# Optimization experiments

Hardware: AMD Instinct MI355X
Metric: run time of the kernel (lower is better)

## Reference

```python
import jax, jax.numpy as jnp
import numpy as np

DIM = 1536
NH = 12
HD = DIM // NH          # 128
C = HD // 2             # 64 rotary pairs
F, H, W = 6, 20, 20
L = F * H * W           # 2400
B = 1
MAX_POS = 1024
EPS = 1e-6


def _rope_freqs():
    """[MAX_POS, C, 2, 2] rotation matrices, split [22,21,21] across f/h/w axes."""
    c0 = C - 2 * (C // 3)           # 22
    c1 = C // 3                      # 21
    pos = np.arange(MAX_POS, dtype=np.float32)
    parts = []
    for m in (c0, c1, c1):
        inv = 1.0 / (10000.0 ** (np.arange(m, dtype=np.float32) / m))
        parts.append(pos[:, None] * inv[None, :])
    ang = np.concatenate(parts, axis=1)          # [MAX_POS, C]
    cos, sin = np.cos(ang), np.sin(ang)
    # R[..., j, k]: rows [cos, -sin], [sin, cos]
    R = np.stack([np.stack([cos, -sin], -1), np.stack([sin, cos], -1)], -2)
    return jnp.asarray(R, dtype=jnp.float32)


def setup_inputs() -> dict:
    key = jax.random.key(0)
    ks = jax.random.split(key, 12)
    s = 1.0 / np.sqrt(DIM)
    lin = lambda k: (jax.random.normal(k, (DIM, DIM), jnp.float32) * s)
    return {
        "x": jax.random.normal(ks[0], (B, L, DIM), jnp.float32),
        "Wq": lin(ks[1]), "bq": jax.random.normal(ks[2], (DIM,), jnp.float32) * 0.01,
        "Wk": lin(ks[3]), "bk": jax.random.normal(ks[4], (DIM,), jnp.float32) * 0.01,
        "Wv": lin(ks[5]), "bv": jax.random.normal(ks[6], (DIM,), jnp.float32) * 0.01,
        "Wo": lin(ks[7]), "bo": jax.random.normal(ks[8], (DIM,), jnp.float32) * 0.01,
        "gq": jnp.ones((DIM,), jnp.float32),
        "gk": jnp.ones((DIM,), jnp.float32),
        "seq_lens": jnp.full((B,), L, dtype=jnp.int32),
        "grid_sizes": jnp.asarray([[F, H, W]], dtype=jnp.int32),
        "freqs": _rope_freqs(),
    }


def _rms_norm(x, g, eps=EPS):
    # WanRMSNorm: x * rsqrt(mean(x^2, -1) + eps) * weight
    return x * jax.lax.rsqrt(jnp.mean(jnp.square(x), axis=-1, keepdims=True) + eps) * g


def _rope_apply(xh, grid_sizes, freqs):
    """xh: [B, L, n, d]; freqs: [MAX_POS, c, 2, 2]. All samples share one grid."""
    b, l, n, d = xh.shape
    c = d // 2
    c0 = c - 2 * (c // 3)
    c1 = c // 3
    f, h, w = (int(v) for v in np.asarray(grid_sizes[0]))
    # build per-position 3D rotation matrices: [f*h*w, c, 2, 2]
    fa = jnp.broadcast_to(freqs[:f, :c0][:, None, None], (f, h, w, c0, 2, 2))
    fb = jnp.broadcast_to(freqs[:h, c0:c0 + c1][None, :, None], (f, h, w, c1, 2, 2))
    fc = jnp.broadcast_to(freqs[:w, c0 + c1:c][None, None, :], (f, h, w, c1, 2, 2))
    R = jnp.concatenate([fa, fb, fc], axis=3).reshape(f * h * w, c, 2, 2)
    xp = xh.reshape(b, l, n, c, 2)
    out = jnp.einsum('lcjk,blnck->blncj', R, xp)
    return out.reshape(b, l, n, d)


def reference(x, Wq, bq, Wk, bk, Wv, bv, Wo, bo, gq, gk, seq_lens, grid_sizes, freqs):
    b, l = x.shape[:2]
    q = _rms_norm(x @ Wq.T + bq, gq).reshape(b, l, NH, HD)
    k = _rms_norm(x @ Wk.T + bk, gk).reshape(b, l, NH, HD)
    v = (x @ Wv.T + bv).reshape(b, l, NH, HD)
    q = _rope_apply(q, grid_sizes, freqs)
    k = _rope_apply(k, grid_sizes, freqs)
    # full attention with key-length mask (window_size=(-1,-1))
    scores = jnp.einsum('bqnd,bknd->bnqk', q, k) / np.sqrt(HD)
    kmask = jnp.arange(l)[None, :] < seq_lens[:, None]          # [B, L]
    scores = jnp.where(kmask[:, None, None, :], scores, -1e9)
    attn = jax.nn.softmax(scores, axis=-1)
    out = jnp.einsum('bnqk,bknd->bqnd', attn, v).reshape(b, l, DIM)
    return out @ Wo.T + bo
```

## Files before the change

### kernel.cpp

```cpp
#include <hip/hip_runtime.h>
#include <hip/hip_bf16.h>
#include <stdint.h>


#define DIM  1536
#define NH   12
#define HD   128
#define LSEQ 2400
#define LPAD 2432
#define KT2  32
#define NT2  (LPAD / KT2)

typedef __attribute__((ext_vector_type(8))) short short8;
typedef __attribute__((ext_vector_type(8))) _Float16 half8;
typedef __attribute__((ext_vector_type(4))) float f32x4;
typedef unsigned short ushort_t;
typedef unsigned int   uint32;

__device__ __forceinline__ ushort_t f2bf(float f) {
  union { float f; unsigned u; } v; v.f = f;
  unsigned r = (v.u + 0x7fffu + ((v.u >> 16) & 1u)) >> 16;
  return (ushort_t)r;
}
__device__ __forceinline__ float bf2f(ushort_t h) {
  union { unsigned u; float f; } v; v.u = ((unsigned)h) << 16;
  return v.f;
}
__device__ __forceinline__ uint32 cvtpk(float lo, float hi) {
  uint32 r;
  asm("v_cvt_pk_bf16_f32 %0, %1, %2" : "=v"(r) : "v"(lo), "v"(hi));
  return r;
}
__device__ __forceinline__ void async16(void* lds, const void* g) {
  __builtin_amdgcn_global_load_lds(
      (const __attribute__((address_space(1))) uint32*)g,
      (__attribute__((address_space(3))) uint32*)lds, 16, 0, 0);
}
__device__ __forceinline__ uint4 pack8(const float* f) {
  uint4 u;
  u.x = (uint32)f2bf(f[0]) | ((uint32)f2bf(f[1]) << 16);
  u.y = (uint32)f2bf(f[2]) | ((uint32)f2bf(f[3]) << 16);
  u.z = (uint32)f2bf(f[4]) | ((uint32)f2bf(f[5]) << 16);
  u.w = (uint32)f2bf(f[6]) | ((uint32)f2bf(f[7]) << 16);
  return u;
}

__global__ void cvt_all(const float* __restrict__ x,
                        const float* __restrict__ W0, const float* __restrict__ W1,
                        const float* __restrict__ W2, const float* __restrict__ W3,
                        ushort_t* __restrict__ xd,
                        ushort_t* __restrict__ d0, ushort_t* __restrict__ d1,
                        ushort_t* __restrict__ d2, ushort_t* __restrict__ d3)
{
  const int z = blockIdx.y;
  const int i = blockIdx.x * 256 + threadIdx.x;
  if (z == 0) {
    uint4 u = {0, 0, 0, 0};
    if (i * 8 < LSEQ * DIM) {
      float f[8];
      *(float4*)f = *(const float4*)(x + i * 8);
      *(float4*)(f + 4) = *(const float4*)(x + i * 8 + 4);
      u = pack8(f);
    }
    *(uint4*)(xd + i * 8) = u;
    return;
  }
  if (blockIdx.x >= DIM * DIM / 2048) return;
  const float* s = (z == 1) ? W0 : ((z == 2) ? W1 : ((z == 3) ? W2 : W3));
  ushort_t* d    = (z == 1) ? d0 : ((z == 2) ? d1 : ((z == 3) ? d2 : d3));
  float f[8];
  *(float4*)f = *(const float4*)(s + i * 8);
  *(float4*)(f + 4) = *(const float4*)(s + i * 8 + 4);
  *(uint4*)(d + i * 8) = pack8(f);
}

__global__ __launch_bounds__(256) void gemm_bt(
    const ushort_t* __restrict__ Ap,
    const ushort_t* __restrict__ B0, const ushort_t* __restrict__ B1, const ushort_t* __restrict__ B2,
    const float* __restrict__ b0, const float* __restrict__ b1, const float* __restrict__ b2,
    ushort_t* __restrict__ D0, ushort_t* __restrict__ D1, ushort_t* __restrict__ D2)
{
  const int z = blockIdx.y;
  const ushort_t* Bw  = (z == 0) ? B0 : ((z == 1) ? B1 : B2);
  const float* bias   = (z == 0) ? b0 : ((z == 1) ? b1 : b2);
  ushort_t* D         = (z == 0) ? D0 : ((z == 1) ? D1 : D2);

  const int bid = blockIdx.x;
  const int x_ = bid & 7, k_ = bid >> 3;
  const int swz = (x_ < 4 ? x_ * 29 : 116 + (x_ - 4) * 28) + k_;
  const int bm = swz / 12, bn = swz % 12;
  const int tid = threadIdx.x;
  const int w = tid >> 6, lam = tid & 63;
  const int wr = w >> 1, wc = w & 1;
  const int lane15 = lam & 15, quad = lam >> 4;

  __shared__ __align__(16) char lds[65536];

  f32x4 acc[4][4];
#pragma unroll
  for (int i = 0; i < 4; ++i)
#pragma unroll
    for (int j = 0; j < 4; ++j) acc[i][j] = {};

  const int sm = (w * 32) + (lam >> 3);
  const int sc = (lam & 7);

#define GSTAGE(k0, buf)                                                       \
  {                                                                           \
    char* sA_ = lds + (buf) * 32768;                                          \
    char* sB_ = lds + (buf) * 32768 + 16384;                                  \
    _Pragma("unroll")                                                         \
    for (int i = 0; i < 4; ++i) {                                             \
      const int li = w * 4096 + i * 1024;                                     \
      const int m = sm + i * 8;                                               \
      const int c = sc ^ (m & 7);                                             \
      async16(sA_ + li, Ap + (size_t)(bm * 128 + m) * DIM + (k0) + c * 8);    \
      async16(sB_ + li, Bw + (size_t)(bn * 128 + m) * DIM + (k0) + c * 8);    \
    }                                                                         \
  }

  GSTAGE(0, 0)
  __syncthreads();

  for (int t = 0; t < DIM / 64; ++t) {
    if (t + 1 < DIM / 64) GSTAGE((t + 1) * 64, (t + 1) & 1)
    const char* sA = lds + (t & 1) * 32768;
    const char* sB = lds + (t & 1) * 32768 + 16384;
#pragma unroll
    for (int kc = 0; kc < 2; ++kc) {
      const int chunk = kc * 4 + quad;
      short8 af[4], bfr[4];
#pragma unroll
      for (int i = 0; i < 4; ++i) {
        const int m = wr * 64 + i * 16 + lane15;
        af[i] = *(const short8*)(sA + m * 128 + ((chunk ^ (m & 7)) * 16));
      }
#pragma unroll
      for (int j = 0; j < 4; ++j) {
        const int n = wc * 64 + j * 16 + lane15;
        bfr[j] = *(const short8*)(sB + n * 128 + ((chunk ^ (n & 7)) * 16));
      }
#pragma unroll
      for (int i = 0; i < 4; ++i)
#pragma unroll
        for (int j = 0; j < 4; ++j)
          acc[i][j] = __builtin_amdgcn_mfma_f32_16x16x32_bf16(af[i], bfr[j], acc[i][j], 0, 0, 0);
    }
    __syncthreads();
  }
#undef GSTAGE

#pragma unroll
  for (int j = 0; j < 4; ++j) {
    const int n = bn * 128 + wc * 64 + j * 16 + lane15;
    const float bv = bias[n];
#pragma unroll
    for (int i = 0; i < 4; ++i) {
      const int mb = bm * 128 + wr * 64 + i * 16 + quad * 4;
#pragma unroll
      for (int r = 0; r < 4; ++r) {
        const int m = mb + r;
        D[(size_t)m * DIM + n] = f2bf(acc[i][j][r] + bv);
      }
    }
  }
}

__global__ __launch_bounds__(256) void gemm_o(
    const ushort_t* __restrict__ Ap, const ushort_t* __restrict__ Bw,
    const float* __restrict__ bias, float* __restrict__ D, int Mout)
{
  const int bid = blockIdx.x;
  const int swz = (bid & 7) * 57 + (bid >> 3);
  const int bm = swz / 12, bn = swz % 12;
  const int tid = threadIdx.x;
  const int w = tid >> 6, lam = tid & 63;
  const int wr = w >> 1, wc = w & 1;
  const int lane15 = lam & 15, quad = lam >> 4;

  __shared__ __align__(16) char lds[49152];

  f32x4 acc[2][4];
#pragma unroll
  for (int i = 0; i < 2; ++i)
#pragma unroll
    for (int j = 0; j < 4; ++j) acc[i][j] = {};

#define OSTAGE(k0, buf)                                                       \
  {                                                                           \
    char* sA_ = lds + (buf) * 24576;                                          \
    char* sB_ = lds + (buf) * 24576 + 8192;                                   \
    _Pragma("unroll")                                                         \
    for (int i = 0; i < 2; ++i) {                                             \
      const int slot = i * 256 + tid;           \
      const int row = slot >> 3;                                              \
      const int c = (slot & 7) ^ (row & 7);                                   \
      async16(sA_ + slot * 16, Ap + (size_t)(bm * 64 + row) * DIM + (k0) + c * 8); \
    }                                                                         \
    _Pragma("unroll")                                                         \
    for (int i = 0; i < 4; ++i) {                                             \
      const int slot = i * 256 + tid;            \
      const int row = slot >> 3;                                              \
      const int c = (slot & 7) ^ (row & 7);                                   \
      async16(sB_ + slot * 16, Bw + (size_t)(bn * 128 + row) * DIM + (k0) + c * 8); \
    }                                                                         \
  }

  OSTAGE(0, 0)
  __syncthreads();

  for (int t = 0; t < DIM / 64; ++t) {
    if (t + 1 < DIM / 64) OSTAGE((t + 1) * 64, (t + 1) & 1)
    const char* sA = lds + (t & 1) * 24576;
    const char* sB = lds + (t & 1) * 24576 + 8192;
#pragma unroll
    for (int kc = 0; kc < 2; ++kc) {
      const int chunk = kc * 4 + quad;
      short8 af[2], bfr[4];
#pragma unroll
      for (int i = 0; i < 2; ++i) {
        const int m = wr * 32 + i * 16 + lane15;
        af[i] = *(const short8*)(sA + m * 128 + ((chunk ^ (m & 7)) * 16));
      }
#pragma unroll
      for (int j = 0; j < 4; ++j) {
        const int n = wc * 64 + j * 16 + lane15;
        bfr[j] = *(const short8*)(sB + n * 128 + ((chunk ^ (n & 7)) * 16));
      }
#pragma unroll
      for (int i = 0; i < 2; ++i)
#pragma unroll
        for (int j = 0; j < 4; ++j)
          acc[i][j] = __builtin_amdgcn_mfma_f32_16x16x32_bf16(af[i], bfr[j], acc[i][j], 0, 0, 0);
    }
    __syncthreads();
  }
#undef OSTAGE

#pragma unroll
  for (int j = 0; j < 4; ++j) {
    const int n = bn * 128 + wc * 64 + j * 16 + lane15;
    const float bv = bias[n];
#pragma unroll
    for (int i = 0; i < 2; ++i) {
      const int mb = bm * 64 + wr * 32 + i * 16 + quad * 4;
#pragma unroll
      for (int r = 0; r < 4; ++r) {
        const int m = mb + r;
        if (m < Mout) D[(size_t)m * DIM + n] = acc[i][j][r] + bv;
      }
    }
  }
}

__global__ __launch_bounds__(256) void nr_vp(
    const ushort_t* __restrict__ qpre, const ushort_t* __restrict__ kpre,
    const ushort_t* __restrict__ vbf,
    const float* __restrict__ gq, const float* __restrict__ gk,
    const float* __restrict__ freqs,
    const int* __restrict__ seq_lens, const int* __restrict__ grid_sizes,
    ushort_t* __restrict__ qh, ushort_t* __restrict__ kh,
    ushort_t* __restrict__ vp)
{
  const int bx = blockIdx.x;
  const int tid = threadIdx.x;
  __shared__ float wsum[4];
  __shared__ float srstd;
  __shared__ ushort_t tbuf[32][33];

  if (bx >= 2 * LPAD) {
    const int vb = bx - 2 * LPAD;
    const int head = vb / (NT2 * 4);
    const int rem = vb - head * (NT2 * 4);
    const int t2 = rem >> 2;
    const int d0 = (rem & 3) * 32;
    const int l0 = t2 * 32;
    const int tx = tid & 31, ty = tid >> 5;
#pragma unroll
    for (int rr = 0; rr < 4; ++rr)
      tbuf[ty * 4 + rr][tx] = vbf[(size_t)(l0 + ty * 4 + rr) * DIM + head * HD + d0 + tx];
    __syncthreads();
    const int tx2 = ((tx >> 2) & 3) * 8 + (tx >> 4) * 4 + (tx & 3);
#pragma unroll
    for (int rr = 0; rr < 4; ++rr) {
      const int d = d0 + ty * 4 + rr;
      vp[(((size_t)head * NT2 + t2) * HD + d) * KT2 + tx2] = tbuf[tx][ty * 4 + rr];
    }
    return;
  }

  const int row = bx >> 1;
  const int which = bx & 1;
  const ushort_t* src = which ? kpre : qpre;
  const float* g = which ? gk : gq;
  ushort_t* dst = which ? kh : qh;

  float s = 0.f;
  if (tid < 192) {
    uint4 u = *(const uint4*)(src + (size_t)row * DIM + tid * 8);
    const uint32 uu[4] = {u.x, u.y, u.z, u.w};
#pragma unroll
    for (int i = 0; i < 4; ++i) {
      float a = bf2f((ushort_t)(uu[i] & 0xffff));
      float b = bf2f((ushort_t)(uu[i] >> 16));
      s += a * a + b * b;
    }
  }
#pragma unroll
  for (int off = 32; off; off >>= 1) s += __shfl_down(s, off, 64);
  if ((tid & 63) == 0) wsum[tid >> 6] = s;
  __syncthreads();
  if (tid == 0)
    srstd = rsqrtf((wsum[0] + wsum[1] + wsum[2] + wsum[3]) / (float)DIM + 1e-6f);
  __syncthreads();
  const float rstd = srstd;

  const int seq = seq_lens[0];
  const int h_ = grid_sizes[1], w_ = grid_sizes[2];
  const int hw = h_ * w_;
  const int fidx = row / hw;
  const int rem = row - fidx * hw;
  const int hidx = rem / w_;
  const int widx = rem - hidx * w_;
  const bool live = row < seq;

#pragma unroll
  for (int pp = 0; pp < 3; ++pp) {
    const int p = tid + pp * 256;
    const int c = p & 63, head = p >> 6;
    const int e_in = head * HD + 2 * c;
    uint32 xin = *(const uint32*)(src + (size_t)row * DIM + e_in);
    float x0 = bf2f((ushort_t)(xin & 0xffff));
    float x1 = bf2f((ushort_t)(xin >> 16));
    float2 gg = *(const float2*)(g + e_in);
    float y0 = x0 * rstd * gg.x, y1 = x1 * rstd * gg.y;
    const int pos = (c < 22) ? fidx : ((c < 43) ? hidx : widx);
    float4 R = *(const float4*)(freqs + ((size_t)pos * 64 + c) * 4);
    float o0 = R.x * y0 + R.y * y1;
    float o1 = R.z * y0 + R.w * y1;
    uint32 op = live ? ((uint32)f2bf(o0) | ((uint32)f2bf(o1) << 16)) : 0u;
    *(uint32*)(dst + ((size_t)head * LPAD + row) * HD + 2 * c) = op;
  }
}

__global__ __launch_bounds__(256, 3) void attn8(
    const ushort_t* __restrict__ qh, const ushort_t* __restrict__ kh,
    const ushort_t* __restrict__ vp, const int* __restrict__ seq_lens,
    _Float16* __restrict__ op0, _Float16* __restrict__ op1,
    _Float16* __restrict__ op2, float* __restrict__ lp)
{
  const int bid = blockIdx.x;
  const int x_ = bid & 7, k_ = bid >> 3;
  const int swz = (x_ < 4 ? x_ * 86 : 344 + (x_ - 4) * 85) + k_;
  const int qz = swz / 228;
  const int rem_ = swz - qz * 228;
  const int head = rem_ / 19;
  const int qx = rem_ - head * 19;
  const int q0 = qx * 128;
  const int tbase = qz * 25;
  const int ntq = 25 + (qz == 2);
  const int tid = threadIdx.x;
  const int w = tid >> 6, lam = tid & 63;
  const int lane15 = lam & 15, quad = lam >> 4;
  const int seq = seq_lens[0];
  _Float16* op = (qz == 0) ? op0 : ((qz == 1) ? op1 : op2);

  __shared__ __align__(16) char kbuf[2][8192];
  __shared__ __align__(16) char vbuf[2][8192];

  const ushort_t* qbase = qh + ((size_t)head * LPAD + q0 + w * 32) * HD;
  short8 qf[2][4];
#pragma unroll
  for (int qt = 0; qt < 2; ++qt)
#pragma unroll
    for (int kc = 0; kc < 4; ++kc)
      qf[qt][kc] = *(const short8*)(qbase + (qt * 16 + lane15) * HD + kc * 32 + quad * 8);

  f32x4 o[2][8];
#pragma unroll
  for (int qt = 0; qt < 2; ++qt)
#pragma unroll
    for (int dt = 0; dt < 8; ++dt) o[qt][dt] = {};
  float lacc[2] = {};

  const float c1 = 0.12751744510848893f;
  const float c2 = 17.312340490667562f;

  const ushort_t* khh = kh + (size_t)head * LPAD * HD;
  const ushort_t* vph = vp + (size_t)head * NT2 * HD * KT2;

  const int krow0 = w * 8 + (lam >> 4);
  const int kslot = lam & 15;

#define STAGE(gt, b)                                                     \
  {                                                                      \
    const ushort_t* kg = khh + (size_t)(gt) * (KT2 * HD);                \
    const ushort_t* vg = vph + (size_t)(gt) * (HD * KT2);                \
    _Pragma("unroll")                                                    \
    for (int i = 0; i < 2; ++i) {                                        \
      const int li = w * 2048 + i * 1024;                                \
      const int kr = krow0 + i * 4;                                      \
      const int kc_ = kslot ^ (kr & 15);                                 \
      async16(kbuf[b] + li, kg + kr * HD + kc_ * 8);                     \
      const int G = w * 128 + i * 64 + lam;                              \
      const int vdt = G >> 6, vdd = (G >> 2) & 15, vqq = G & 3;          \
      async16(vbuf[b] + li, vg + (vdt * 16 + vdd) * KT2 + vqq * 8);      \
    }                                                                    \
  }

  STAGE(tbase, 0)
  __syncthreads();

  for (int t = 0; t < ntq; ++t) {
    const int b = t & 1;
    const int gt = tbase + t;
    if (t + 1 < ntq) STAGE(gt + 1, b ^ 1)

    f32x4 S[2][2];
    S[0][0] = {}; S[0][1] = {}; S[1][0] = {}; S[1][1] = {};
#pragma unroll
    for (int n0 = 0; n0 < 2; ++n0)
#pragma unroll
      for (int kc = 0; kc < 4; ++kc) {
        short8 kf = *(const short8*)(kbuf[b] + (n0 * 16 + lane15) * 256 +
                                     (((kc * 4 + quad) ^ lane15) * 16));
#pragma unroll
        for (int qt = 0; qt < 2; ++qt)
          S[qt][n0] = __builtin_amdgcn_mfma_f32_16x16x32_bf16(kf, qf[qt][kc], S[qt][n0], 0, 0, 0);
      }

    const bool edge = (gt + 1) * KT2 > seq;
    short8 pa8[2];
#pragma unroll
    for (int qt = 0; qt < 2; ++qt) {
      float ev[8];
#pragma unroll
      for (int n0 = 0; n0 < 2; ++n0)
#pragma unroll
        for (int r = 0; r < 4; ++r)
          ev[n0 * 4 + r] = exp2f(S[qt][n0][r] * c1 - c2);
      if (edge) {
#pragma unroll
        for (int n0 = 0; n0 < 2; ++n0) {
          const int kb0 = gt * KT2 + n0 * 16 + quad * 4;
#pragma unroll
          for (int r = 0; r < 4; ++r)
            if (kb0 + r >= seq) ev[n0 * 4 + r] = 0.f;
        }
      }
      float s8 = ((ev[0] + ev[1]) + (ev[2] + ev[3])) +
                 ((ev[4] + ev[5]) + (ev[6] + ev[7]));
      lacc[qt] += s8;
      union { uint32 u[4]; short8 s; } pk;
      pk.u[0] = cvtpk(ev[0], ev[1]);
      pk.u[1] = cvtpk(ev[2], ev[3]);
      pk.u[2] = cvtpk(ev[4], ev[5]);
      pk.u[3] = cvtpk(ev[6], ev[7]);
      pa8[qt] = pk.s;
    }

#pragma unroll
    for (int dt = 0; dt < 8; ++dt) {
      short8 vf = *(const short8*)(vbuf[b] + dt * 1024 + lane15 * 64 + quad * 16);
#pragma unroll
      for (int qt = 0; qt < 2; ++qt)
        o[qt][dt] = __builtin_amdgcn_mfma_f32_16x16x32_bf16(pa8[qt], vf, o[qt][dt], 0, 0, 0);
    }
    __syncthreads();
  }
#undef STAGE

#pragma unroll
  for (int qt = 0; qt < 2; ++qt) {
    float l = lacc[qt];
    l += __shfl_xor(l, 16, 64);
    l += __shfl_xor(l, 32, 64);
    if (lam < 16)
      lp[((size_t)qz * NH + head) * LPAD + q0 + w * 32 + qt * 16 + lam] = l;
    const float lrcp = 1.0f / l;
    float linv[4];
#pragma unroll
    for (int r = 0; r < 4; ++r) linv[r] = __shfl(lrcp, quad * 4 + r, 64);
#pragma unroll
    for (int dt = 0; dt < 8; ++dt)
#pragma unroll
      for (int r = 0; r < 4; ++r) {
        const int m = q0 + w * 32 + qt * 16 + quad * 4 + r;
        op[(size_t)m * DIM + head * HD + dt * 16 + lane15] =
            (_Float16)(o[qt][dt][r] * linv[r]);
      }
  }
}

__global__ void merge(const _Float16* __restrict__ o0, const _Float16* __restrict__ o1,
                      const _Float16* __restrict__ o2,
                      const float* __restrict__ lp, ushort_t* __restrict__ attno)
{
  const int i = blockIdx.x * 256 + threadIdx.x;
  const int e = i * 8;
  const int m = e / DIM;
  const int head = (e - m * DIM) >> 7;
  float l[3];
#pragma unroll
  for (int h = 0; h < 3; ++h) l[h] = lp[((size_t)h * NH + head) * LPAD + m];
  const float inv = 1.0f / (l[0] + l[1] + l[2]);
  half8 a = *(const half8*)(o0 + e);
  half8 b = *(const half8*)(o1 + e);
  half8 c = *(const half8*)(o2 + e);
  const float w0 = l[0] * inv, w1 = l[1] * inv, w2 = l[2] * inv;
  float f[8];
#pragma unroll
  for (int j = 0; j < 8; ++j)
    f[j] = (float)a[j] * w0 + (float)b[j] * w1 + (float)c[j] * w2;
  *(uint4*)(attno + e) = pack8(f);
}

extern "C" void kernel_launch(void* const* d_in, const int* in_sizes, int n_in,
                              void* d_out, int out_size, void* d_ws, size_t ws_size,
                              hipStream_t stream)
{
  const float* x  = (const float*)d_in[0];
  const float* Wq = (const float*)d_in[1];
  const float* bq = (const float*)d_in[2];
  const float* Wk = (const float*)d_in[3];
  const float* bk = (const float*)d_in[4];
  const float* Wv = (const float*)d_in[5];
  const float* bv = (const float*)d_in[6];
  const float* Wo = (const float*)d_in[7];
  const float* bo = (const float*)d_in[8];
  const float* gq = (const float*)d_in[9];
  const float* gk = (const float*)d_in[10];
  const int* seq_lens   = (const int*)d_in[11];
  const int* grid_sizes = (const int*)d_in[12];
  const float* freqs    = (const float*)d_in[13];
  float* out = (float*)d_out;

  const size_t BUF = (size_t)LPAD * DIM * 2;
  const size_t WB  = (size_t)DIM * DIM * 2;
  char* ws = (char*)d_ws;
  dim3 blk(256);

  ushort_t* xbf  = (ushort_t*)(ws);
  ushort_t* wqb  = (ushort_t*)(ws + BUF);
  ushort_t* wkb  = (ushort_t*)(ws + BUF + WB);
  ushort_t* wvb  = (ushort_t*)(ws + BUF + 2 * WB);
  ushort_t* wob  = (ushort_t*)(ws + BUF + 3 * WB);
  ushort_t* qpre = (ushort_t*)(ws + BUF + 4 * WB);
  ushort_t* kpre = (ushort_t*)(ws + 2 * BUF + 4 * WB);
  ushort_t* qh   = (ushort_t*)(ws + 3 * BUF + 4 * WB);
  ushort_t* kh   = (ushort_t*)(ws + 4 * BUF + 4 * WB);
  ushort_t* vbf  = (ushort_t*)(ws + 5 * BUF + 4 * WB);
  ushort_t* vp    = xbf;
  ushort_t* attno = xbf;
  _Float16* op0 = (_Float16*)qpre;
  _Float16* op1 = (_Float16*)kpre;
  _Float16* op2 = (_Float16*)vbf;
  float*    lp  = (float*)wvb;

  cvt_all<<<dim3(LPAD * DIM / 2048, 5), blk, 0, stream>>>(
      x, Wq, Wk, Wv, Wo, xbf, wqb, wkb, wvb, wob);
  gemm_bt<<<dim3(228, 3), blk, 0, stream>>>(
      xbf, wqb, wkb, wvb, bq, bk, bv, qpre, kpre, vbf);
  nr_vp<<<dim3(2 * LPAD + NH * NT2 * 4), blk, 0, stream>>>(
      qpre, kpre, vbf, gq, gk, freqs, seq_lens, grid_sizes, qh, kh, vp);
  attn8<<<dim3(684), blk, 0, stream>>>(
      qh, kh, vp, seq_lens, op0, op1, op2, lp);
  merge<<<dim3(LPAD * DIM / 2048), blk, 0, stream>>>(op0, op1, op2, lp, attno);
  gemm_o<<<dim3(456), blk, 0, stream>>>(attno, wob, bo, out, LSEQ);
}
```

Measured before the change: 263.5 us.

## Fuse split-K attention merge into output projection GEMM A-tile loading

After: 271.5 us. 3.0% more time.

```diff
diff --git a/kernel.cpp b/kernel.cpp
--- a/kernel.cpp
+++ b/kernel.cpp
@@ -166,9 +166,11 @@
   }
 }
 
-__global__ __launch_bounds__(256) void gemm_o(
-    const ushort_t* __restrict__ Ap, const ushort_t* __restrict__ Bw,
-    const float* __restrict__ bias, float* __restrict__ D, int Mout)
+__global__ __launch_bounds__(256) void gemm_om(
+    const _Float16* __restrict__ A0, const _Float16* __restrict__ A1,
+    const _Float16* __restrict__ A2, const float* __restrict__ lp,
+    const ushort_t* __restrict__ Bw, const float* __restrict__ bias,
+    float* __restrict__ D, int Mout)
 {
   const int bid = blockIdx.x;
   const int swz = (bid & 7) * 57 + (bid >> 3);
@@ -186,31 +188,67 @@
 #pragma unroll
     for (int j = 0; j < 4; ++j) acc[i][j] = {};
 
-#define OSTAGE(k0, buf)                                                       \
+  half8 ra[2], rb[2], rc[2];
+  float l0v[2], l1v[2], l2v[2];
+
+#define OLOADA(k0)                                                            \
+  {                                                                           \
+    _Pragma("unroll")                                                         \
+    for (int i = 0; i < 2; ++i) {                                             \
+      const int slot = i * 256 + tid;                                         \
+      const int row = slot >> 3;                                              \
+      const int c = (slot & 7) ^ (row & 7);                                   \
+      const int k = (k0) + c * 8;                                             \
+      const int head = k >> 7;                                                \
+      const int gr = bm * 64 + row;                                           \
+      ra[i] = *(const half8*)(A0 + (size_t)gr * DIM + k);                     \
+      rb[i] = *(const half8*)(A1 + (size_t)gr * DIM + k);                     \
+      rc[i] = *(const half8*)(A2 + (size_t)gr * DIM + k);                     \
+      l0v[i] = lp[(size_t)head * LPAD + gr];                                  \
+      l1v[i] = lp[(size_t)(NH + head) * LPAD + gr];                           \
+      l2v[i] = lp[(size_t)(2 * NH + head) * LPAD + gr];                       \
+    }                                                                         \
+  }
+
+#define OWRITEA(buf)                                                          \
   {                                                                           \
     char* sA_ = lds + (buf) * 24576;                                          \
+    _Pragma("unroll")                                                         \
+    for (int i = 0; i < 2; ++i) {                                             \
+      const int slot = i * 256 + tid;                                         \
+      const float inv = 1.0f / (l0v[i] + l1v[i] + l2v[i]);                    \
+      const float w0 = l0v[i] * inv, w1 = l1v[i] * inv, w2 = l2v[i] * inv;    \
+      float f[8];                                                             \
+      _Pragma("unroll")                                                       \
+      for (int j = 0; j < 8; ++j)                                             \
+        f[j] = (float)ra[i][j] * w0 + (float)rb[i][j] * w1 +                  \
+               (float)rc[i][j] * w2;                                          \
+      uint4 u;                                                                \
+      u.x = cvtpk(f[0], f[1]); u.y = cvtpk(f[2], f[3]);                       \
+      u.z = cvtpk(f[4], f[5]); u.w = cvtpk(f[6], f[7]);                       \
+      *(uint4*)(sA_ + slot * 16) = u;                                         \
+    }                                                                         \
+  }
+
+#define OSTAGEB(k0, buf)                                                      \
+  {                                                                           \
     char* sB_ = lds + (buf) * 24576 + 8192;                                   \
     _Pragma("unroll")                                                         \
-    for (int i = 0; i < 2; ++i) {                                             \
-      const int slot = i * 256 + tid;           \
-      const int row = slot >> 3;                                              \
-      const int c = (slot & 7) ^ (row & 7);                                   \
-      async16(sA_ + slot * 16, Ap + (size_t)(bm * 64 + row) * DIM + (k0) + c * 8); \
-    }                                                                         \
-    _Pragma("unroll")                                                         \
     for (int i = 0; i < 4; ++i) {                                             \
-      const int slot = i * 256 + tid;            \
+      const int slot = i * 256 + tid;                                         \
       const int row = slot >> 3;                                              \
       const int c = (slot & 7) ^ (row & 7);                                   \
       async16(sB_ + slot * 16, Bw + (size_t)(bn * 128 + row) * DIM + (k0) + c * 8); \
     }                                                                         \
   }
 
-  OSTAGE(0, 0)
+  OLOADA(0)
+  OSTAGEB(0, 0)
+  OWRITEA(0)
   __syncthreads();
 
   for (int t = 0; t < DIM / 64; ++t) {
-    if (t + 1 < DIM / 64) OSTAGE((t + 1) * 64, (t + 1) & 1)
+    if (t + 1 < DIM / 64) OLOADA((t + 1) * 64)
     const char* sA = lds + (t & 1) * 24576;
     const char* sB = lds + (t & 1) * 24576 + 8192;
 #pragma unroll
@@ -233,9 +271,15 @@
         for (int j = 0; j < 4; ++j)
           acc[i][j] = __builtin_amdgcn_mfma_f32_16x16x32_bf16(af[i], bfr[j], acc[i][j], 0, 0, 0);
     }
+    if (t + 1 < DIM / 64) {
+      OSTAGEB((t + 1) * 64, (t + 1) & 1);
+      OWRITEA((t + 1) & 1);
+    }
     __syncthreads();
   }
-#undef OSTAGE
+#undef OLOADA
+#undef OWRITEA
+#undef OSTAGEB
 
 #pragma unroll
   for (int j = 0; j < 4; ++j) {
@@ -492,29 +536,6 @@
   }
 }
 
-__global__ void merge(const _Float16* __restrict__ o0, const _Float16* __restrict__ o1,
-                      const _Float16* __restrict__ o2,
-                      const float* __restrict__ lp, ushort_t* __restrict__ attno)
-{
-  const int i = blockIdx.x * 256 + threadIdx.x;
-  const int e = i * 8;
-  const int m = e / DIM;
-  const int head = (e - m * DIM) >> 7;
-  float l[3];
-#pragma unroll
-  for (int h = 0; h < 3; ++h) l[h] = lp[((size_t)h * NH + head) * LPAD + m];
-  const float inv = 1.0f / (l[0] + l[1] + l[2]);
-  half8 a = *(const half8*)(o0 + e);
-  half8 b = *(const half8*)(o1 + e);
-  half8 c = *(const half8*)(o2 + e);
-  const float w0 = l[0] * inv, w1 = l[1] * inv, w2 = l[2] * inv;
-  float f[8];
-#pragma unroll
-  for (int j = 0; j < 8; ++j)
-    f[j] = (float)a[j] * w0 + (float)b[j] * w1 + (float)c[j] * w2;
-  *(uint4*)(attno + e) = pack8(f);
-}
-
 extern "C" void kernel_launch(void* const* d_in, const int* in_sizes, int n_in,
                               void* d_out, int out_size, void* d_ws, size_t ws_size,
                               hipStream_t stream)
@@ -551,7 +572,6 @@
   ushort_t* kh   = (ushort_t*)(ws + 4 * BUF + 4 * WB);
   ushort_t* vbf  = (ushort_t*)(ws + 5 * BUF + 4 * WB);
   ushort_t* vp    = xbf;
-  ushort_t* attno = xbf;
   _Float16* op0 = (_Float16*)qpre;
   _Float16* op1 = (_Float16*)kpre;
   _Float16* op2 = (_Float16*)vbf;
@@ -565,6 +585,6 @@
       qpre, kpre, vbf, gq, gk, freqs, seq_lens, grid_sizes, qh, kh, vp);
   attn8<<<dim3(684), blk, 0, stream>>>(
       qh, kh, vp, seq_lens, op0, op1, op2, lp);
-  merge<<<dim3(LPAD * DIM / 2048), blk, 0, stream>>>(op0, op1, op2, lp, attno);
-  gemm_o<<<dim3(456), blk, 0, stream>>>(attno, wob, bo, out, LSEQ);
-}
+  gemm_om<<<dim3(456), blk, 0, stream>>>(
+      op0, op1, op2, lp, wob, bo, out, LSEQ);
+}
```
